# Kernel optimization log

Hardware: AMD Instinct MI355X
Metric: run time of the kernel (lower is better)

The kernel has to match this reference:

```python
import itertools
import jax, jax.numpy as jnp
import numpy as np

N = 6          # particles per spin channel -> 720 permutations
D = 3          # spatial dim
HID = 64
BATCH = 2048


def _perms_and_signs(n):
    """All n! permutations in lexicographic order + their signs (+1/-1)."""
    perms = np.array(list(itertools.permutations(range(n))), dtype=np.int32)
    i, j = np.triu_indices(n, 1)
    inversions = (perms[:, i] > perms[:, j]).sum(axis=1)
    signs = np.where(inversions % 2 == 0, 1.0, -1.0).astype(np.float32)
    return jnp.asarray(perms), jnp.asarray(signs)


def setup_inputs() -> dict:
    key = jax.random.key(0)
    ks = jax.random.split(key, 6)
    scale1 = 1.0 / np.sqrt(N * D)
    scale2 = 1.0 / np.sqrt(HID)
    return {
        "x1": jax.random.normal(ks[0], (BATCH, N, D), dtype=jnp.float32),
        "x2": jax.random.normal(ks[1], (BATCH, N, D), dtype=jnp.float32),
        "W1a": jax.random.normal(ks[2], (N * D, HID), dtype=jnp.float32) * scale1,
        "b1a": jnp.zeros((HID,), dtype=jnp.float32),
        "W2a": jax.random.normal(ks[3], (HID, 1), dtype=jnp.float32) * scale2,
        "b2a": jnp.zeros((1,), dtype=jnp.float32),
        "W1b": jax.random.normal(ks[4], (N * D, HID), dtype=jnp.float32) * scale1,
        "b1b": jnp.zeros((HID,), dtype=jnp.float32),
        "W2b": jax.random.normal(ks[5], (HID, 1), dtype=jnp.float32) * scale2,
        "b2b": jnp.zeros((1,), dtype=jnp.float32),
    }


def _antisymmetrized_leaf(x, W1, b1, W2, b2):
    # x: (B, n, d). Gather all n! permutations along axis -2.
    n, d = x.shape[-2], x.shape[-1]
    perms, signs = _perms_and_signs(n)          # (n!, n), (n!,)
    x_perm = jnp.take(x, perms, axis=-2)        # (B, n!, n, d)
    x_perm = x_perm.reshape(x_perm.shape[:-2] + (n * d,))  # (B, n!, n*d)
    # fn_to_antisymmetrize: MLP (..., n*d) -> (..., 1)
    h = jnp.tanh(x_perm @ W1 + b1)              # (B, n!, HID)
    perms_out = h @ W2 + b2                     # (B, n!, 1)
    signed = signs[:, None] * perms_out         # (B, n!, 1)
    return jnp.sum(signed, axis=(-1, -2))       # (B,)


def reference(x1, x2, W1a, b1a, W2a, b2a, W1b, b1b, W2b, b2b):
    psi1 = _antisymmetrized_leaf(x1, W1a, b1a, W2a, b2a)
    psi2 = _antisymmetrized_leaf(x2, W1b, b1b, W2b, b2b)
    # logabs=True: sum_i log|psi_i|
    return jnp.log(jnp.abs(psi1)) + jnp.log(jnp.abs(psi2))
```

## Files before the change

### kernel.cpp

```cpp
#include <hip/hip_runtime.h>
#include <math.h>


__device__ __forceinline__ float fexp2(float x) {
#if __has_builtin(__builtin_amdgcn_exp2f)
    return __builtin_amdgcn_exp2f(x);
#else
    return exp2f(x);
#endif
}
__device__ __forceinline__ float frcp(float x) {
#if __has_builtin(__builtin_amdgcn_rcpf)
    return __builtin_amdgcn_rcpf(x);
#else
    return 1.0f / x;
#endif
}

constexpr int lowest_free(unsigned used) {
    for (int j = 0; j < 6; ++j)
        if (!(used & (1u << j))) return j;
    return -1;
}

template <int LVL, unsigned USED, int PAR>
struct Node {
    template <int J>
    static __device__ __forceinline__ void step(const float (&F)[6][6],
                                                const float (&t)[6][6], float P,
                                                double& acc) {
        if constexpr ((USED & (1u << J)) == 0) {
            constexpr int par2 = PAR ^ (__builtin_popcount(USED >> (J + 1)) & 1);
            if constexpr (LVL == 0)
                Node<1, (1u << J), par2>::go(F, t, F[J][0], acc);
            else
                Node<LVL + 1, USED | (1u << J), par2>::go(F, t, P * F[J][LVL], acc);
        }
    }
    static __device__ __forceinline__ void go(const float (&F)[6][6],
                                              const float (&t)[6][6], float P,
                                              double& acc) {
        step<0>(F, t, P, acc);
        step<1>(F, t, P, acc);
        step<2>(F, t, P, acc);
        step<3>(F, t, P, acc);
        step<4>(F, t, P, acc);
        step<5>(F, t, P, acc);
    }
};

template <unsigned USED, int PAR>
struct Node<4, USED, PAR> {
    static __device__ __forceinline__ void go(const float (&F)[6][6],
                                              const float (&t)[6][6], float P,
                                              double& acc) {
        constexpr int a = lowest_free(USED);
        constexpr int b = lowest_free(USED | (1u << a));
        constexpr int inv_a = __builtin_popcount(USED >> (a + 1));
        constexpr int inv_b = __builtin_popcount((USED | (1u << a)) >> (b + 1));
        constexpr int par_ab = PAR ^ ((inv_a + inv_b) & 1);

        float Ea = P * t[a][b];
        float Eb = P * t[b][a];
        float num = Eb - Ea;
        float den = (Ea + 1.0f) * (Eb + 1.0f);
        float d = num * frcp(den);
        if constexpr (par_ab == 0) acc += (double)d;
        else                       acc -= (double)d;
    }
};

__global__ __launch_bounds__(256, 4) void antisym_kernel(
    const float* __restrict__ x1, const float* __restrict__ x2,
    const float* __restrict__ W1a, const float* __restrict__ b1a,
    const float* __restrict__ W2a,
    const float* __restrict__ W1b, const float* __restrict__ b1b,
    const float* __restrict__ W2b,
    float* __restrict__ out, int B) {
    __shared__ float lds_log[4];

    const int lane = threadIdx.x & 63;
    const int wave = threadIdx.x >> 6;
    const int b = blockIdx.x * 2 + (wave >> 1);
    const int ch = wave & 1;

    if (b < B) {
        const float* x  = ch ? x2  : x1;
        const float* W1 = ch ? W1b : W1a;
        const float* b1 = ch ? b1b : b1a;
        const float* W2 = ch ? W2b : W2a;

        const float K = 2.8853900817779268f;

        float w1c[18];
#pragma unroll
        for (int r = 0; r < 18; ++r) w1c[r] = W1[r * 64 + lane] * K;
        const float b1s = b1[lane] * K;
        const float w2v = W2[lane];

        float xv[18];
        const float* xb = x + b * 18;
#pragma unroll
        for (int r = 0; r < 18; ++r) xv[r] = xb[r];

        float F[6][6];
#pragma unroll
        for (int j = 0; j < 6; ++j)
#pragma unroll
            for (int i = 0; i < 6; ++i) {
                float c = xv[j * 3 + 0] * w1c[i * 3 + 0] +
                          xv[j * 3 + 1] * w1c[i * 3 + 1] +
                          xv[j * 3 + 2] * w1c[i * 3 + 2];
                if (i == 0) c += b1s;
                F[j][i] = fexp2(c);
            }

        float t[6][6];
#pragma unroll
        for (int a = 0; a < 6; ++a)
#pragma unroll
            for (int bb = 0; bb < 6; ++bb)
                if (a != bb) t[a][bb] = F[a][4] * F[bb][5];

        double acc = 0.0;
        Node<0, 0u, 0>::go(F, t, 1.0f, acc);

        double v = (double)w2v * acc * -2.0;
#pragma unroll
        for (int off = 32; off > 0; off >>= 1) v += __shfl_xor(v, off, 64);

        if (lane == 0) lds_log[wave] = logf(fabsf((float)v));
    }
    __syncthreads();
    if (threadIdx.x < 2) {
        int bb = blockIdx.x * 2 + threadIdx.x;
        if (bb < B)
            out[bb] = lds_log[threadIdx.x * 2] + lds_log[threadIdx.x * 2 + 1];
    }
}

extern "C" void kernel_launch(void* const* d_in, const int* in_sizes, int n_in,
                              void* d_out, int out_size, void* d_ws, size_t ws_size,
                              hipStream_t stream) {
    const float* x1  = (const float*)d_in[0];
    const float* x2  = (const float*)d_in[1];
    const float* W1a = (const float*)d_in[2];
    const float* b1a = (const float*)d_in[3];
    const float* W2a = (const float*)d_in[4];
    const float* W1b = (const float*)d_in[6];
    const float* b1b = (const float*)d_in[7];
    const float* W2b = (const float*)d_in[8];

    const int B = in_sizes[0] / 18;
    float* out = (float*)d_out;

    dim3 grid((B + 1) / 2), block(256);
    hipLaunchKernelGGL(antisym_kernel, grid, block, 0, stream,
                       x1, x2, W1a, b1a, W2a, W1b, b1b, W2b, out, B);
}
```

Baseline: 100.5 us.

## Collapse last three permutation levels into one combined rational per leaf

Stops the permutation recursion at level 3 and handles the three remaining children together. It uses precomputed pairwise tables (difference, sum and product of the exp terms), so each leaf group forms three quadratic denominators and combines them into a single fraction with one reciprocal and one double-precision accumulate instead of three. This cuts reciprocals and fp64 adds per group of six permutations and splits the result across two double accumulators to shorten the dependency chain. In exchange there are more float multiplies, and a product of three denominators could overflow or lose precision for large activations.

```diff
diff --git a/kernel.cpp b/kernel.cpp
--- a/kernel.cpp
+++ b/kernel.cpp
@@ -23,50 +23,76 @@
     return -1;
 }
 
+struct Tbl {
+    float F[6][4];
+    float w[6][6];
+    float s[6][6];
+    float q[6][6];
+};
+
 template <int LVL, unsigned USED, int PAR>
 struct Node {
     template <int J>
-    static __device__ __forceinline__ void step(const float (&F)[6][6],
-                                                const float (&t)[6][6], float P,
-                                                double& acc) {
+    static __device__ __forceinline__ void step(const Tbl& T, float P,
+                                                double& a0, double& a1) {
         if constexpr ((USED & (1u << J)) == 0) {
             constexpr int par2 = PAR ^ (__builtin_popcount(USED >> (J + 1)) & 1);
             if constexpr (LVL == 0)
-                Node<1, (1u << J), par2>::go(F, t, F[J][0], acc);
+                Node<1, (1u << J), par2>::go(T, T.F[J][0], a0, a1);
             else
-                Node<LVL + 1, USED | (1u << J), par2>::go(F, t, P * F[J][LVL], acc);
+                Node<LVL + 1, USED | (1u << J), par2>::go(T, P * T.F[J][LVL], a0, a1);
         }
     }
-    static __device__ __forceinline__ void go(const float (&F)[6][6],
-                                              const float (&t)[6][6], float P,
-                                              double& acc) {
-        step<0>(F, t, P, acc);
-        step<1>(F, t, P, acc);
-        step<2>(F, t, P, acc);
-        step<3>(F, t, P, acc);
-        step<4>(F, t, P, acc);
-        step<5>(F, t, P, acc);
+    static __device__ __forceinline__ void go(const Tbl& T, float P,
+                                              double& a0, double& a1) {
+        step<0>(T, P, a0, a1);
+        step<1>(T, P, a0, a1);
+        step<2>(T, P, a0, a1);
+        step<3>(T, P, a0, a1);
+        step<4>(T, P, a0, a1);
+        step<5>(T, P, a0, a1);
     }
 };
 
 template <unsigned USED, int PAR>
-struct Node<4, USED, PAR> {
-    static __device__ __forceinline__ void go(const float (&F)[6][6],
-                                              const float (&t)[6][6], float P,
-                                              double& acc) {
-        constexpr int a = lowest_free(USED);
-        constexpr int b = lowest_free(USED | (1u << a));
-        constexpr int inv_a = __builtin_popcount(USED >> (a + 1));
-        constexpr int inv_b = __builtin_popcount((USED | (1u << a)) >> (b + 1));
-        constexpr int par_ab = PAR ^ ((inv_a + inv_b) & 1);
+struct Node<3, USED, PAR> {
+    template <int X, int A, int B>
+    static __device__ __forceinline__ float child_den(const Tbl& T, float P3,
+                                                      float& n) {
+        float P4 = P3 * T.F[X][3];
+        float Q  = P4 * P4;
+        n = P4 * T.w[A][B];
+        return fmaf(Q, T.q[A][B], fmaf(P4, T.s[A][B], 1.0f));
+    }
+    template <int X, int A, int B>
+    static constexpr int child_sign() {
+        constexpr unsigned U4 = USED | (1u << X);
+        constexpr int inv_x = __builtin_popcount(USED >> (X + 1));
+        constexpr int inv_a = __builtin_popcount(U4 >> (A + 1));
+        constexpr int inv_b = __builtin_popcount((U4 | (1u << A)) >> (B + 1));
+        return (PAR ^ ((inv_x + inv_a + inv_b) & 1));
+    }
+    static __device__ __forceinline__ void go(const Tbl& T, float P3,
+                                              double& a0, double& a1) {
+        constexpr int x0 = lowest_free(USED);
+        constexpr int x1 = lowest_free(USED | (1u << x0));
+        constexpr int x2 = lowest_free(USED | (1u << x0) | (1u << x1));
+        constexpr float sg0 = child_sign<x0, x1, x2>() ? -1.0f : 1.0f;
+        constexpr float sg1 = child_sign<x1, x0, x2>() ? -1.0f : 1.0f;
+        constexpr float sg2 = child_sign<x2, x0, x1>() ? -1.0f : 1.0f;
 
-        float Ea = P * t[a][b];
-        float Eb = P * t[b][a];
-        float num = Eb - Ea;
-        float den = (Ea + 1.0f) * (Eb + 1.0f);
-        float d = num * frcp(den);
-        if constexpr (par_ab == 0) acc += (double)d;
-        else                       acc -= (double)d;
+        float n0, n1, n2;
+        float den0 = child_den<x0, x1, x2>(T, P3, n0);
+        float den1 = child_den<x1, x0, x2>(T, P3, n1);
+        float den2 = child_den<x2, x0, x1>(T, P3, n2);
+
+        float d01 = den0 * den1;
+        float den = d01 * den2;
+        float t01 = (sg0 * n0) * den1 + (sg1 * n1) * den0;
+        float num = t01 * den2 + (sg2 * n2) * d01;
+        float r = num * frcp(den);
+        if constexpr (USED & 1) a1 += (double)r;
+        else                    a0 += (double)r;
     }
 };
 
@@ -103,29 +129,38 @@
 #pragma unroll
         for (int r = 0; r < 18; ++r) xv[r] = xb[r];
 
-        float F[6][6];
+        Tbl T;
+        float F4[6], F5[6], g[6];
 #pragma unroll
-        for (int j = 0; j < 6; ++j)
+        for (int j = 0; j < 6; ++j) {
 #pragma unroll
             for (int i = 0; i < 6; ++i) {
                 float c = xv[j * 3 + 0] * w1c[i * 3 + 0] +
                           xv[j * 3 + 1] * w1c[i * 3 + 1] +
                           xv[j * 3 + 2] * w1c[i * 3 + 2];
                 if (i == 0) c += b1s;
-                F[j][i] = fexp2(c);
+                float e = fexp2(c);
+                if (i < 4) T.F[j][i] = e;
+                else if (i == 4) F4[j] = e;
+                else F5[j] = e;
             }
-
-        float t[6][6];
+            g[j] = F4[j] * F5[j];
+        }
 #pragma unroll
         for (int a = 0; a < 6; ++a)
 #pragma unroll
-            for (int bb = 0; bb < 6; ++bb)
-                if (a != bb) t[a][bb] = F[a][4] * F[bb][5];
+            for (int bb = a + 1; bb < 6; ++bb) {
+                float u = F4[a] * F5[bb];
+                float v = F4[bb] * F5[a];
+                T.w[a][bb] = v - u;
+                T.s[a][bb] = u + v;
+                T.q[a][bb] = g[a] * g[bb];
+            }
 
-        double acc = 0.0;
-        Node<0, 0u, 0>::go(F, t, 1.0f, acc);
+        double acc0 = 0.0, acc1 = 0.0;
+        Node<0, 0u, 0>::go(T, 1.0f, acc0, acc1);
 
-        double v = (double)w2v * acc * -2.0;
+        double v = (double)w2v * (acc0 + acc1) * -2.0;
 #pragma unroll
         for (int off = 32; off > 0; off >>= 1) v += __shfl_xor(v, off, 64);
 
```

Measured after the change: 96.74 us. -3.7%, faster.
